# Optimization experiments

Measured on AMD Instinct MI355X. Metric: run time of the kernel, lower is better.

## Reference

```python
import jax, jax.numpy as jnp
import numpy as np


def _chamfer(x1, x2):
    # x1: [B,N,3], x2: [B,M,3]
    # squared pairwise distances via ||a||^2 + ||b||^2 - 2 a.b (fused, no [B,N,M,3] diff tensor)
    n1 = jnp.sum(x1 * x1, axis=-1)                     # [B,N]
    n2 = jnp.sum(x2 * x2, axis=-1)                     # [B,M]
    cross = jnp.einsum('bnd,bmd->bnm', x1, x2)         # [B,N,M]
    d = n1[:, :, None] + n2[:, None, :] - 2.0 * cross  # [B,N,M]
    d = jnp.maximum(d, 0.0)
    dist1 = jnp.min(d, axis=2)  # [B,N] nearest in x2 for each x1 point
    dist2 = jnp.min(d, axis=1)  # [B,M] nearest in x1 for each x2 point
    return dist1, dist2


def setup_inputs() -> dict:
    key = jax.random.key(0)
    k1, k2 = jax.random.split(key)
    B, N, M, D = 16, 4096, 4096, 3
    input1 = jax.random.normal(k1, (B, N, D), dtype=jnp.float32)
    input2 = jax.random.normal(k2, (B, M, D), dtype=jnp.float32)
    return {"input1": input1, "input2": input2}


def reference(input1, input2):
    return _chamfer(input1, input2)
```

## Files before the change

kernel.cpp:

```cpp
#include <hip/hip_runtime.h>


#define CB 16
#define CN 4096
#define CM 4096
#define WVS 8
#define NQT 2
#define QPW (NQT * 16)
#define QPB (WVS * QPW)
#define TPC 2048
#define NCH (CM / TPC)
#define NTT (TPC / 16)

typedef float f32x4 __attribute__((ext_vector_type(4)));
typedef short bf16x8 __attribute__((ext_vector_type(8)));
typedef unsigned int u32;
typedef u32 u32x4 __attribute__((ext_vector_type(4)));
typedef float v4f __attribute__((ext_vector_type(4)));

__device__ __forceinline__ u32 pack2(float a, float b) {
    return __builtin_amdgcn_perm(__float_as_uint(b), __float_as_uint(a),
                                 0x07060302u);
}
__device__ __forceinline__ float hi_f(float a) {
    return __uint_as_float(__float_as_uint(a) & 0xFFFF0000u);
}

__global__ __launch_bounds__(512, 4) void chamfer_mfma(
    const float* __restrict__ x1, const float* __restrict__ x2,
    float* __restrict__ out)
{
    const int dir   = blockIdx.z;
    const int b     = blockIdx.y;
    const int qtile = blockIdx.x;

    const float* __restrict__ qraw = (dir ? x2 : x1) + (size_t)b * CN * 3;
    const float* __restrict__ traw = (dir ? x1 : x2) + (size_t)b * CM * 3;
    float* __restrict__ o = out + (dir ? ((size_t)CB * CN + (size_t)b * CM)
                                       : ((size_t)b * CN)) + qtile * QPB;

    __shared__ u32x4 AI[NTT * 32];

    const int tid  = threadIdx.x;
    const int lane = tid & 63;
    const int wave = __builtin_amdgcn_readfirstlane(tid >> 6);
    const int col  = lane & 15;
    const int kb   = lane >> 4;

    bf16x8 bq[NQT];
    float nq[NQT];
    #pragma unroll
    for (int qt = 0; qt < NQT; ++qt) {
        const float* qp = qraw
            + (size_t)3 * (qtile * QPB + wave * QPW + qt * 16 + col);
        float qx = qp[0], qy = qp[1], qz = qp[2];
        nq[qt] = fmaf(qx, qx, fmaf(qy, qy, qz * qz));
        float MX = -2.f * qx, MY = -2.f * qy, MZ = -2.f * qz;
        float mxl = MX - hi_f(MX);
        float myl = MY - hi_f(MY);
        float mzl = MZ - hi_f(MZ);
        u32x4 w;
        if (kb == 0)
            w = (u32x4){pack2(MX, MY), pack2(MZ, MX),
                        pack2(MY, MZ), pack2(mxl, myl)};
        else if (kb == 1)
            w = (u32x4){pack2(mzl, 1.0f), pack2(1.0f, 0.f), 0u, 0u};
        else
            w = (u32x4){0u, 0u, 0u, 0u};
        bq[qt] = __builtin_bit_cast(bf16x8, w);
    }

    float best0[NQT], best1[NQT];
    #pragma unroll
    for (int qt = 0; qt < NQT; ++qt) { best0[qt] = 1e30f; best1[qt] = 1e30f; }

    const int lsel = lane & 31;
    #pragma unroll 1
    for (int c = 0; c < NCH; ++c) {
        {
            const v4f* rv = (const v4f*)(traw + (size_t)(c * TPC + 4 * tid) * 3);
            v4f r0 = rv[0], r1 = rv[1], r2 = rv[2];
            const float tx[4] = {r0.x, r0.w, r1.z, r2.y};
            const float ty[4] = {r0.y, r1.x, r1.w, r2.z};
            const float tz[4] = {r0.z, r1.y, r2.x, r2.w};
            #pragma unroll
            for (int i = 0; i < 4; ++i) {
                float X = tx[i], Y = ty[i], Zc = tz[i];
                float xl = X - hi_f(X);
                float yl = Y - hi_f(Y);
                float zl = Zc - hi_f(Zc);
                float nt = fmaf(X, X, fmaf(Y, Y, Zc * Zc));
                float ntl = nt - hi_f(nt);
                const int r = 4 * tid + i;
                const int base = (r >> 4) * 32 + (r & 15);
                AI[base +  0] = (u32x4){pack2(X, Y), pack2(Zc, xl),
                                        pack2(yl, zl), pack2(X, Y)};
                AI[base + 16] = (u32x4){pack2(Zc, nt), pack2(ntl, 0.f),
                                        0u, 0u};
            }
        }
        __syncthreads();

        #pragma unroll 1
        for (int t = 0; t < NTT; t += 4) {
            #pragma unroll
            for (int u = 0; u < 4; ++u) {
                bf16x8 af = __builtin_bit_cast(bf16x8, AI[(t + u) * 32 + lsel]);
                #pragma unroll
                for (int qt = 0; qt < NQT; ++qt) {
                    f32x4 acc = __builtin_amdgcn_mfma_f32_16x16x32_bf16(
                        af, bq[qt], (f32x4){0.f, 0.f, 0.f, 0.f}, 0, 0, 0);
                    best0[qt] = fminf(fminf(best0[qt], acc.x), acc.y);
                    best1[qt] = fminf(fminf(best1[qt], acc.z), acc.w);
                }
            }
        }
        __syncthreads();
    }

    #pragma unroll
    for (int qt = 0; qt < NQT; ++qt) {
        float v = fminf(best0[qt], best1[qt]);
        v = fminf(v, __shfl_xor(v, 16));
        v = fminf(v, __shfl_xor(v, 32));
        if (kb == 0)
            o[wave * QPW + qt * 16 + col] = fmaxf(v + nq[qt], 0.f);
    }
}

extern "C" void kernel_launch(void* const* d_in, const int* in_sizes, int n_in,
                              void* d_out, int out_size, void* d_ws, size_t ws_size,
                              hipStream_t stream) {
    const float* x1 = (const float*)d_in[0];
    const float* x2 = (const float*)d_in[1];
    float* out = (float*)d_out;

    chamfer_mfma<<<dim3(16, CB, 2), 512, 0, stream>>>(x1, x2, out);
}
```

Measured before the change: 78.09 us.

## Split target set across blocks, double queries per wave, merge via atomicMin

Each block now handles 512 queries (four 16-query tiles per wave) against half of the target points, with the two halves combined through an unsigned-integer atomicMin on the non-negative float results. An init kernel fills the output with +inf first. This removes the per-block loop over two target chunks and its extra barrier, and raises MFMA reuse of each LDS A-fragment across more query tiles. The cost is an extra kernel launch, atomic traffic and higher register pressure from the larger query tile count.

```diff
diff --git a/kernel.cpp b/kernel.cpp
--- a/kernel.cpp
+++ b/kernel.cpp
@@ -5,12 +5,11 @@
 #define CN 4096
 #define CM 4096
 #define WVS 8
-#define NQT 2
+#define NQT 4
 #define QPW (NQT * 16)
 #define QPB (WVS * QPW)
-#define TPC 2048
-#define NCH (CM / TPC)
-#define NTT (TPC / 16)
+#define TPH 2048
+#define NTT (TPH / 16)
 
 typedef float f32x4 __attribute__((ext_vector_type(4)));
 typedef short bf16x8 __attribute__((ext_vector_type(8)));
@@ -26,18 +25,25 @@
     return __uint_as_float(__float_as_uint(a) & 0xFFFF0000u);
 }
 
+__global__ void init_out(unsigned* __restrict__ out)
+{
+    out[blockIdx.x * 512 + threadIdx.x] = 0x7F800000u;
+}
+
 __global__ __launch_bounds__(512, 4) void chamfer_mfma(
     const float* __restrict__ x1, const float* __restrict__ x2,
-    float* __restrict__ out)
+    unsigned* __restrict__ out)
 {
     const int dir   = blockIdx.z;
     const int b     = blockIdx.y;
-    const int qtile = blockIdx.x;
+    const int qtile = blockIdx.x & 7;
+    const int thalf = blockIdx.x >> 3;
 
     const float* __restrict__ qraw = (dir ? x2 : x1) + (size_t)b * CN * 3;
-    const float* __restrict__ traw = (dir ? x1 : x2) + (size_t)b * CM * 3;
-    float* __restrict__ o = out + (dir ? ((size_t)CB * CN + (size_t)b * CM)
-                                       : ((size_t)b * CN)) + qtile * QPB;
+    const float* __restrict__ traw = (dir ? x1 : x2) + (size_t)b * CM * 3
+                                   + (size_t)thalf * TPH * 3;
+    unsigned* __restrict__ o = out + (dir ? ((size_t)CB * CN + (size_t)b * CM)
+                                          : ((size_t)b * CN)) + qtile * QPB;
 
     __shared__ u32x4 AI[NTT * 32];
 
@@ -46,6 +52,29 @@
     const int wave = __builtin_amdgcn_readfirstlane(tid >> 6);
     const int col  = lane & 15;
     const int kb   = lane >> 4;
+    const int lsel = lane & 31;
+
+    {
+        const v4f* rv = (const v4f*)(traw + (size_t)12 * tid);
+        v4f r0 = rv[0], r1 = rv[1], r2 = rv[2];
+        const float tx[4] = {r0.x, r0.w, r1.z, r2.y};
+        const float ty[4] = {r0.y, r1.x, r1.w, r2.z};
+        const float tz[4] = {r0.z, r1.y, r2.x, r2.w};
+        #pragma unroll
+        for (int i = 0; i < 4; ++i) {
+            float X = tx[i], Y = ty[i], Zc = tz[i];
+            float xl = X - hi_f(X);
+            float yl = Y - hi_f(Y);
+            float zl = Zc - hi_f(Zc);
+            float nt = fmaf(X, X, fmaf(Y, Y, Zc * Zc));
+            float ntl = nt - hi_f(nt);
+            const int r = 4 * tid + i;
+            const int base = (r >> 4) * 32 + (r & 15);
+            AI[base +  0] = (u32x4){pack2(X, Y), pack2(Zc, xl),
+                                    pack2(yl, zl), pack2(X, Y)};
+            AI[base + 16] = (u32x4){pack2(Zc, nt), pack2(ntl, 0.f), 0u, 0u};
+        }
+    }
 
     bf16x8 bq[NQT];
     float nq[NQT];
@@ -74,48 +103,21 @@
     #pragma unroll
     for (int qt = 0; qt < NQT; ++qt) { best0[qt] = 1e30f; best1[qt] = 1e30f; }
 
-    const int lsel = lane & 31;
+    __syncthreads();
+
     #pragma unroll 1
-    for (int c = 0; c < NCH; ++c) {
-        {
-            const v4f* rv = (const v4f*)(traw + (size_t)(c * TPC + 4 * tid) * 3);
-            v4f r0 = rv[0], r1 = rv[1], r2 = rv[2];
-            const float tx[4] = {r0.x, r0.w, r1.z, r2.y};
-            const float ty[4] = {r0.y, r1.x, r1.w, r2.z};
-            const float tz[4] = {r0.z, r1.y, r2.x, r2.w};
+    for (int t = 0; t < NTT; t += 2) {
+        #pragma unroll
+        for (int u = 0; u < 2; ++u) {
+            bf16x8 af = __builtin_bit_cast(bf16x8, AI[(t + u) * 32 + lsel]);
             #pragma unroll
-            for (int i = 0; i < 4; ++i) {
-                float X = tx[i], Y = ty[i], Zc = tz[i];
-                float xl = X - hi_f(X);
-                float yl = Y - hi_f(Y);
-                float zl = Zc - hi_f(Zc);
-                float nt = fmaf(X, X, fmaf(Y, Y, Zc * Zc));
-                float ntl = nt - hi_f(nt);
-                const int r = 4 * tid + i;
-                const int base = (r >> 4) * 32 + (r & 15);
-                AI[base +  0] = (u32x4){pack2(X, Y), pack2(Zc, xl),
-                                        pack2(yl, zl), pack2(X, Y)};
-                AI[base + 16] = (u32x4){pack2(Zc, nt), pack2(ntl, 0.f),
-                                        0u, 0u};
+            for (int qt = 0; qt < NQT; ++qt) {
+                f32x4 acc = __builtin_amdgcn_mfma_f32_16x16x32_bf16(
+                    af, bq[qt], (f32x4){0.f, 0.f, 0.f, 0.f}, 0, 0, 0);
+                best0[qt] = fminf(fminf(best0[qt], acc.x), acc.y);
+                best1[qt] = fminf(fminf(best1[qt], acc.z), acc.w);
             }
         }
-        __syncthreads();
-
-        #pragma unroll 1
-        for (int t = 0; t < NTT; t += 4) {
-            #pragma unroll
-            for (int u = 0; u < 4; ++u) {
-                bf16x8 af = __builtin_bit_cast(bf16x8, AI[(t + u) * 32 + lsel]);
-                #pragma unroll
-                for (int qt = 0; qt < NQT; ++qt) {
-                    f32x4 acc = __builtin_amdgcn_mfma_f32_16x16x32_bf16(
-                        af, bq[qt], (f32x4){0.f, 0.f, 0.f, 0.f}, 0, 0, 0);
-                    best0[qt] = fminf(fminf(best0[qt], acc.x), acc.y);
-                    best1[qt] = fminf(fminf(best1[qt], acc.z), acc.w);
-                }
-            }
-        }
-        __syncthreads();
     }
 
     #pragma unroll
@@ -123,8 +125,10 @@
         float v = fminf(best0[qt], best1[qt]);
         v = fminf(v, __shfl_xor(v, 16));
         v = fminf(v, __shfl_xor(v, 32));
-        if (kb == 0)
-            o[wave * QPW + qt * 16 + col] = fmaxf(v + nq[qt], 0.f);
+        if (kb == 0) {
+            float val = fmaxf(v + nq[qt], 0.f);
+            atomicMin(o + wave * QPW + qt * 16 + col, __float_as_uint(val));
+        }
     }
 }
 
@@ -133,7 +137,8 @@
                               hipStream_t stream) {
     const float* x1 = (const float*)d_in[0];
     const float* x2 = (const float*)d_in[1];
-    float* out = (float*)d_out;
+    unsigned* out = (unsigned*)d_out;
 
+    init_out<<<dim3(2 * CB * CN / 512), 512, 0, stream>>>(out);
     chamfer_mfma<<<dim3(16, CB, 2), 512, 0, stream>>>(x1, x2, out);
 }
```

Measured after the change: 78.57 us. No clear change (+0.6%).
